# Optimization experiments

Measured on AMD Instinct MI355X. Metric: run time of the kernel, lower is better.

Reference implementation:

```python
import jax, jax.numpy as jnp
import numpy as np

B, S, H, E, V, OOV = 64, 400, 512, 256, 50000, 100

def setup_inputs() -> dict:
    key = jax.random.key(0)
    ks = jax.random.split(key, 32)
    p = lambda i, shape: jax.random.normal(ks[i], shape, jnp.float32) * 0.02
    emb = p(0, (V, E)).at[0].set(0.0)  # padding_idx=0
    return dict(
        summaries_in=jax.random.randint(ks[1], (B,), 1, V),
        h0=jax.random.normal(ks[2], (B, H), jnp.float32),
        c0=jax.random.normal(ks[3], (B, H), jnp.float32),
        encoder_out=jax.random.normal(ks[4], (B, S, 2 * H), jnp.float32),
        encoder_features=jax.random.normal(ks[5], (S * B, 2 * H), jnp.float32),
        encoder_mask=jnp.ones((S, B), jnp.float32),
        context=jax.random.normal(ks[6], (B, 2 * H), jnp.float32),
        coverage=jax.random.uniform(ks[7], (S, B), jnp.float32) * 0.01,
        texts_extended=jax.random.randint(ks[8], (S, B), 0, V + OOV),
        oov_size=OOV,
        emb=emb,
        W_feat=p(10, (2 * H, 2 * H)), b_feat=p(11, (2 * H,)),
        W_cov=p(12, (2 * H,)), b_cov=p(13, (2 * H,)),
        w_att=p(14, (2 * H,)), b_att=p(15, ()),
        W_ih=p(16, (4 * H, E)), W_hh=p(17, (4 * H, H)),
        b_ih=p(18, (4 * H,)), b_hh=p(19, (4 * H,)),
        W_ctx=p(20, (E, 2 * H + E)), b_ctx=p(21, (E,)),
        W_pg=p(22, (4 * H + E,)), b_pg=p(23, ()),
        W_o1=p(24, (H, 3 * H)), b_o1=p(25, (H,)),
        W_o2=p(26, (V, H)), b_o2=p(27, (V,)),
    )


def reference(summaries_in, h0, c0, encoder_out, encoder_features, encoder_mask,
              context, coverage, texts_extended, oov_size, emb,
              W_feat, b_feat, W_cov, b_cov, w_att, b_att,
              W_ih, W_hh, b_ih, b_hh, W_ctx, b_ctx, W_pg, b_pg,
              W_o1, b_o1, W_o2, b_o2):
    # embedding + context projection: [B, 2H+E] -> [B, E]
    x = emb[summaries_in]
    ctx_out = jnp.concatenate([context, x], axis=1) @ W_ctx.T + b_ctx
    # single LSTM step (torch gate order i, f, g, o)
    gates = ctx_out @ W_ih.T + b_ih + h0 @ W_hh.T + b_hh
    i, f, g, o = jnp.split(gates, 4, axis=1)
    c = jax.nn.sigmoid(f) * c0 + jax.nn.sigmoid(i) * jnp.tanh(g)
    h = jax.nn.sigmoid(o) * jnp.tanh(c)
    hidden_out = jnp.concatenate([h, c], axis=1)  # [B, 2H]
    # Bahdanau attention with coverage
    dec_feat = hidden_out @ W_feat.T + b_feat                 # [B, 2H]
    ef = encoder_features.reshape(S, B, 2 * H)                # [S, B, 2H]
    cov_feat = coverage[..., None] * W_cov + b_cov            # Linear(1, 2H)
    e = jnp.tanh(ef + dec_feat[None] + cov_feat) @ w_att + b_att  # [S, B]
    a = jax.nn.softmax(e, axis=0) * encoder_mask
    a = a / jnp.sum(a, axis=0, keepdims=True)                 # renormalize (Normalize(0))
    ctx_new = jnp.einsum('sb,bsd->bd', a, encoder_out)        # [B, 2H]
    coverage_next = coverage + a
    # pointer-generator mix
    gen_in = jnp.concatenate([ctx_new, hidden_out, ctx_out], axis=1)  # [B, 4H+E]
    p_gen = jax.nn.sigmoid(gen_in @ W_pg + b_pg)[:, None]             # [B, 1]
    logits = (jnp.concatenate([h, ctx_new], axis=1) @ W_o1.T + b_o1) @ W_o2.T + b_o2
    vocab_dist = p_gen * jax.nn.softmax(logits, axis=1)       # [B, V]
    attn_w = (1.0 - p_gen) * a.T                              # [B, S]
    vd = jnp.concatenate([vocab_dist, jnp.zeros((B, oov_size), vocab_dist.dtype)], axis=1)
    vd = vd.at[jnp.arange(B)[:, None], texts_extended.T].add(attn_w)  # scatter_add copy dist
    return vd, hidden_out, ctx_new, a, coverage_next
```

## Files before the change

kernel.cpp:

```cpp
#include <hip/hip_runtime.h>
#include <cmath>

#define B 64
#define S 400
#define H 512
#define E 256
#define V 50000
#define OOV 100
#define H2 1024
#define VDN (V + OOV)
#define NBLK_V 782

typedef __attribute__((ext_vector_type(8))) short short8;
typedef __attribute__((ext_vector_type(4))) float f32x4;

__device__ __forceinline__ float wred_sum(float v) {
#pragma unroll
  for (int o = 32; o > 0; o >>= 1) v += __shfl_down(v, o, 64);
  return v;
}
__device__ __forceinline__ float wred_max(float v) {
#pragma unroll
  for (int o = 32; o > 0; o >>= 1) v = fmaxf(v, __shfl_down(v, o, 64));
  return v;
}
__device__ __forceinline__ short f2bf(float f) {
  return __builtin_bit_cast(short, (__bf16)f);
}

__global__ __launch_bounds__(256) void k_init(const float* __restrict__ b_ctx,
                                              const float* __restrict__ b_ih,
                                              const float* __restrict__ b_hh,
                                              const float* __restrict__ b_feat,
                                              const float* __restrict__ b_o1,
                                              float* __restrict__ ctxoutT4,
                                              float* __restrict__ gates,
                                              float* __restrict__ dfeat,
                                              float* __restrict__ innerT4) {
  int idx = blockIdx.x * 256 + threadIdx.x;
  if (idx < 16384) {
    int j = ((idx >> 8) << 2) + (idx & 3);
    ctxoutT4[idx] = b_ctx[j];
  } else if (idx < 16384 + 131072) {
    int i = idx - 16384;
    int j = i & 2047;
    gates[i] = b_ih[j] + b_hh[j];
  } else if (idx < 16384 + 131072 + 65536) {
    int i = idx - 16384 - 131072;
    dfeat[i] = b_feat[i & 1023];
  } else {
    int i = idx - 16384 - 131072 - 65536;
    int j = ((i >> 8) << 2) + (i & 3);
    innerT4[i] = b_o1[j];
  }
}

__global__ __launch_bounds__(256) void k_pack(const float* __restrict__ context,
                                              const float* __restrict__ emb,
                                              const int* __restrict__ sumin,
                                              const float* __restrict__ h0,
                                              float* __restrict__ catT4,
                                              float* __restrict__ h0T4) {
  int idx = blockIdx.x * 256 + threadIdx.x;
  if (idx < 81920) {
    int e = idx & 3, b = (idx >> 2) & 63, q = idx >> 8;
    int k = q * 4 + e;
    catT4[idx] = (k < 1024) ? context[b * 1024 + k]
                            : emb[(size_t)sumin[b] * 256 + (k - 1024)];
  } else {
    int i = idx - 81920;
    int e = i & 3, b = (i >> 2) & 63, q = i >> 8;
    h0T4[i] = h0[b * 512 + q * 4 + e];
  }
}

template <int R, int KC, int OUTMODE>
__global__ __launch_bounds__(256) void k_gemmsk(
    const float* __restrict__ A1, const float* __restrict__ W1, int ldw1, int s1,
    const float* __restrict__ A2, const float* __restrict__ W2, int ldw2,
    float* __restrict__ out, int ldout) {
  const int lane = threadIdx.x;
  const int w = threadIdx.y;
  const int j0 = blockIdx.x * (4 * R) + w * R;
  const float* A;
  const float* W;
  int ldw, kc0;
  if ((int)blockIdx.y < s1) {
    A = A1; W = W1; ldw = ldw1; kc0 = blockIdx.y * KC;
  } else {
    A = A2; W = W2; ldw = ldw2; kc0 = (blockIdx.y - s1) * KC;
  }
  float acc[R];
#pragma unroll
  for (int r = 0; r < R; ++r) acc[r] = 0.f;
  const float* ap = A + (size_t)kc0 * 256 + lane * 4;
  const float* wr[R];
#pragma unroll
  for (int r = 0; r < R; ++r) wr[r] = W + (size_t)(j0 + r) * ldw + kc0 * 4;
#pragma unroll 8
  for (int k4 = 0; k4 < KC; ++k4) {
    float4 av = *(const float4*)(ap + (size_t)k4 * 256);
#pragma unroll
    for (int r = 0; r < R; ++r) {
      float4 wv = *(const float4*)(wr[r] + k4 * 4);
      acc[r] += av.x * wv.x + av.y * wv.y + av.z * wv.z + av.w * wv.w;
    }
  }
#pragma unroll
  for (int r = 0; r < R; ++r) {
    int j = j0 + r;
    if constexpr (OUTMODE == 0)
      atomicAdd(&out[((size_t)(j >> 2) * 64 + lane) * 4 + (j & 3)], acc[r]);
    else
      atomicAdd(&out[(size_t)lane * ldout + j], acc[r]);
  }
}

__global__ __launch_bounds__(256) void k_lstm(const float* __restrict__ gates,
                                              const float* __restrict__ c0,
                                              float* __restrict__ hidden,
                                              float* __restrict__ hcT4) {
  int idx = blockIdx.x * 256 + threadIdx.x;
  int b = idx >> 9, u = idx & 511;
  float gi = gates[(size_t)b * 2048 + u];
  float gf = gates[(size_t)b * 2048 + 512 + u];
  float gg = gates[(size_t)b * 2048 + 1024 + u];
  float go = gates[(size_t)b * 2048 + 1536 + u];
  float si = 1.f / (1.f + expf(-gi));
  float sf = 1.f / (1.f + expf(-gf));
  float so = 1.f / (1.f + expf(-go));
  float c = sf * c0[(size_t)b * 512 + u] + si * tanhf(gg);
  float h = so * tanhf(c);
  hidden[(size_t)b * H2 + u] = h;
  hidden[(size_t)b * H2 + 512 + u] = c;
  hcT4[((u >> 2) * 64 + b) * 4 + (u & 3)] = h;
  int k = 512 + u;
  hcT4[((k >> 2) * 64 + b) * 4 + (k & 3)] = c;
}

__global__ __launch_bounds__(128) void k_e(
    const float* __restrict__ ef, const float* __restrict__ dfeat,
    const float* __restrict__ cov, const float* __restrict__ Wcov,
    const float* __restrict__ bcov, const float* __restrict__ watt,
    const float* __restrict__ batt, float* __restrict__ e_out) {
  const int sb = blockIdx.x;
  const int b = sb & 63;
  const float cval = cov[sb];
  const float4* efr = (const float4*)(ef + (size_t)sb * H2);
  const float4* dfr = (const float4*)(dfeat + (size_t)b * H2);
  const float4* wcr = (const float4*)Wcov;
  const float4* bcr = (const float4*)bcov;
  const float4* war = (const float4*)watt;
  float sum = 0.f;
#pragma unroll
  for (int i = 0; i < 2; ++i) {
    int d4 = threadIdx.x + i * 128;
    float4 ev = efr[d4], dv = dfr[d4], wc = wcr[d4], bc = bcr[d4], wa = war[d4];
    sum += tanhf(ev.x + dv.x + cval * wc.x + bc.x) * wa.x;
    sum += tanhf(ev.y + dv.y + cval * wc.y + bc.y) * wa.y;
    sum += tanhf(ev.z + dv.z + cval * wc.z + bc.z) * wa.z;
    sum += tanhf(ev.w + dv.w + cval * wc.w + bc.w) * wa.w;
  }
  sum = wred_sum(sum);
  __shared__ float ls[2];
  if ((threadIdx.x & 63) == 0) ls[threadIdx.x >> 6] = sum;
  __syncthreads();
  if (threadIdx.x == 0) e_out[sb] = ls[0] + ls[1] + batt[0];
}

__global__ __launch_bounds__(512) void k_soft(const float* __restrict__ e,
                                              const float* __restrict__ mask,
                                              const float* __restrict__ cov_in,
                                              float* __restrict__ a_out,
                                              float* __restrict__ cov_out) {
  const int b = blockIdx.x;
  const int s = threadIdx.x;
  __shared__ float red[8];
  float ev = (s < S) ? e[s * B + b] : -INFINITY;
  float m = wred_max(ev);
  if ((s & 63) == 0) red[s >> 6] = m;
  __syncthreads();
  if (s == 0) {
    float mm = red[0];
#pragma unroll
    for (int i = 1; i < 8; ++i) mm = fmaxf(mm, red[i]);
    red[0] = mm;
  }
  __syncthreads();
  m = red[0];
  float ex = (s < S) ? mask[s * B + b] * expf(ev - m) : 0.f;
  float ws = wred_sum(ex);
  __syncthreads();
  if ((s & 63) == 0) red[s >> 6] = ws;
  __syncthreads();
  if (s == 0) {
    float z = 0.f;
#pragma unroll
    for (int i = 0; i < 8; ++i) z += red[i];
    red[0] = z;
  }
  __syncthreads();
  float Z = red[0];
  if (s < S) {
    float av = ex / Z;
    a_out[s * B + b] = av;
    cov_out[s * B + b] = cov_in[s * B + b] + av;
  }
}

__global__ __launch_bounds__(256) void k_ctxp(const float* __restrict__ a,
                                              const float* __restrict__ enc,
                                              float* __restrict__ part) {
  const int b = blockIdx.x & 63;
  const int sc = blockIdx.x >> 6;
  const int d = threadIdx.x * 4;
  float4 acc = make_float4(0.f, 0.f, 0.f, 0.f);
  for (int s = sc * 25; s < sc * 25 + 25; ++s) {
    float av = a[s * B + b];
    float4 ev = *(const float4*)(enc + ((size_t)b * S + s) * H2 + d);
    acc.x += av * ev.x;
    acc.y += av * ev.y;
    acc.z += av * ev.z;
    acc.w += av * ev.w;
  }
  *(float4*)(part + (size_t)blockIdx.x * H2 + d) = acc;
}

__global__ __launch_bounds__(256) void k_ctxred(const float* __restrict__ part,
                                                float* __restrict__ ctx_new,
                                                float* __restrict__ ctxT4) {
  int idx = blockIdx.x * 256 + threadIdx.x;
  float s = 0.f;
#pragma unroll
  for (int sc = 0; sc < 16; ++sc) s += part[(size_t)sc * 65536 + idx];
  int b = idx >> 10, d = idx & 1023;
  ctx_new[idx] = s;
  ctxT4[((d >> 2) * 64 + b) * 4 + (d & 3)] = s;
}

__global__ __launch_bounds__(256) void k_pgen(
    const float* __restrict__ ctx_new, const float* __restrict__ hidden,
    const float* __restrict__ ctxoutT4, const float* __restrict__ Wpg,
    const float* __restrict__ bpg, float* __restrict__ pgen) {
  const int b = blockIdx.x;
  float p = 0.f;
  for (int k = threadIdx.x; k < 2304; k += 256) {
    float v;
    if (k < 1024) v = ctx_new[(size_t)b * H2 + k];
    else if (k < 2048) v = hidden[(size_t)b * H2 + k - 1024];
    else {
      int ko = k - 2048;
      v = ctxoutT4[((ko >> 2) * 64 + b) * 4 + (ko & 3)];
    }
    p += v * Wpg[k];
  }
  p = wred_sum(p);
  __shared__ float red[4];
  if ((threadIdx.x & 63) == 0) red[threadIdx.x >> 6] = p;
  __syncthreads();
  if (threadIdx.x == 0) {
    float d = red[0] + red[1] + red[2] + red[3] + bpg[0];
    pgen[b] = 1.f / (1.f + expf(-d));
  }
}

__global__ __launch_bounds__(256) void k_packinner(const float* __restrict__ innerT4,
                                                   short8* __restrict__ packB) {
  int f = blockIdx.x * 256 + threadIdx.x;
  int l = f & 63, bt = (f >> 6) & 3, ks = f >> 8;
  int b = bt * 16 + (l & 15);
  int kbase = ks * 32 + (l >> 4) * 8;
  float4 q0 = *(const float4*)&innerT4[(size_t)(kbase / 4) * 256 + b * 4];
  float4 q1 = *(const float4*)&innerT4[(size_t)(kbase / 4 + 1) * 256 + b * 4];
  short8 frag;
  frag[0] = f2bf(q0.x); frag[1] = f2bf(q0.y);
  frag[2] = f2bf(q0.z); frag[3] = f2bf(q0.w);
  frag[4] = f2bf(q1.x); frag[5] = f2bf(q1.y);
  frag[6] = f2bf(q1.z); frag[7] = f2bf(q1.w);
  packB[f] = frag;
}

__global__ __launch_bounds__(256) void k_mfma_logits(
    const float* __restrict__ W2, const short8* __restrict__ packB,
    const float* __restrict__ bias, float* __restrict__ logits,
    float* __restrict__ mp, float* __restrict__ zp) {
  const int l = threadIdx.x;
  const int w = threadIdx.y;
  const int jblk = blockIdx.x * 64;
  const int jw = jblk + w * 16;
  const int jv = min(jw + (l & 15), V - 1);
  const float* wp = W2 + (size_t)jv * 512 + (l >> 4) * 8;

  f32x4 acc0 = {0.f, 0.f, 0.f, 0.f}, acc1 = acc0, acc2 = acc0, acc3 = acc0;
#pragma unroll 2
  for (int ks = 0; ks < 16; ++ks) {
    float4 w0 = *(const float4*)&wp[ks * 32];
    float4 w1 = *(const float4*)&wp[ks * 32 + 4];
    short8 af;
    af[0] = f2bf(w0.x); af[1] = f2bf(w0.y); af[2] = f2bf(w0.z); af[3] = f2bf(w0.w);
    af[4] = f2bf(w1.x); af[5] = f2bf(w1.y); af[6] = f2bf(w1.z); af[7] = f2bf(w1.w);
    short8 b0 = packB[(ks * 4 + 0) * 64 + l];
    short8 b1 = packB[(ks * 4 + 1) * 64 + l];
    short8 b2 = packB[(ks * 4 + 2) * 64 + l];
    short8 b3 = packB[(ks * 4 + 3) * 64 + l];
    acc0 = __builtin_amdgcn_mfma_f32_16x16x32_bf16(af, b0, acc0, 0, 0, 0);
    acc1 = __builtin_amdgcn_mfma_f32_16x16x32_bf16(af, b1, acc1, 0, 0, 0);
    acc2 = __builtin_amdgcn_mfma_f32_16x16x32_bf16(af, b2, acc2, 0, 0, 0);
    acc3 = __builtin_amdgcn_mfma_f32_16x16x32_bf16(af, b3, acc3, 0, 0, 0);
  }

  __shared__ float tile[64][65];
  const int rbase = w * 16 + (l >> 4) * 4;
#pragma unroll
  for (int v = 0; v < 4; ++v) {
    int jl = rbase + v;
    int j = jblk + jl;
    float bv = bias[min(j, V - 1)];
    bool valid = (j < V);
    tile[jl][0 * 16 + (l & 15)] = valid ? acc0[v] + bv : -INFINITY;
    tile[jl][1 * 16 + (l & 15)] = valid ? acc1[v] + bv : -INFINITY;
    tile[jl][2 * 16 + (l & 15)] = valid ? acc2[v] + bv : -INFINITY;
    tile[jl][3 * 16 + (l & 15)] = valid ? acc3[v] + bv : -INFINITY;
  }
  __syncthreads();
  const int t = w * 64 + l;
#pragma unroll
  for (int i = 0; i < 16; ++i) {
    int idx = i * 256 + t;
    int jl = idx & 63;
    int b = idx >> 6;
    int j = jblk + jl;
    if (j < V) logits[(size_t)b * V + j] = tile[jl][b];
  }
  if (t < 64) {
    float m = -INFINITY;
#pragma unroll
    for (int jl = 0; jl < 64; ++jl) m = fmaxf(m, tile[jl][t]);
    float z = 0.f;
#pragma unroll
    for (int jl = 0; jl < 64; ++jl) z += expf(tile[jl][t] - m);
    mp[(size_t)blockIdx.x * 64 + t] = m;
    zp[(size_t)blockIdx.x * 64 + t] = z;
  }
}

__global__ __launch_bounds__(256) void k_vdm(const float* __restrict__ logits,
                                             const float* __restrict__ mp,
                                             const float* __restrict__ zp,
                                             const float* __restrict__ pgen,
                                             float* __restrict__ out) {
  const int b = blockIdx.x >> 3;
  const int c = blockIdx.x & 7;
  const int t = threadIdx.x;
  __shared__ float red[4];
  float m = -INFINITY;
  for (int i = t; i < NBLK_V; i += 256) m = fmaxf(m, mp[i * 64 + b]);
  m = wred_max(m);
  if ((t & 63) == 0) red[t >> 6] = m;
  __syncthreads();
  const float M = fmaxf(fmaxf(red[0], red[1]), fmaxf(red[2], red[3]));
  float z = 0.f;
  for (int i = t; i < NBLK_V; i += 256) z += zp[i * 64 + b] * expf(mp[i * 64 + b] - M);
  z = wred_sum(z);
  __syncthreads();
  if ((t & 63) == 0) red[t >> 6] = z;
  __syncthreads();
  const float Z = red[0] + red[1] + red[2] + red[3];
  const float scale = pgen[b] / Z;
  const int v0 = c * 6272;
  const int v1 = min(v0 + 6272, VDN);
  for (int v = v0 + t; v < v1; v += 256) {
    float val = (v < V) ? scale * expf(logits[(size_t)b * V + v] - M) : 0.f;
    out[(size_t)b * VDN + v] = val;
  }
}

__global__ __launch_bounds__(256) void k_scatter(const float* __restrict__ a,
                                                 const int* __restrict__ tex,
                                                 const float* __restrict__ pgen,
                                                 float* __restrict__ vd) {
  int g = blockIdx.x * 256 + threadIdx.x;
  if (g >= S * B) return;
  int b = g & 63;
  float w = (1.f - pgen[b]) * a[g];
  atomicAdd(&vd[(size_t)b * VDN + tex[g]], w);
}

extern "C" void kernel_launch(void* const* d_in, const int* in_sizes, int n_in,
                              void* d_out, int out_size, void* d_ws, size_t ws_size,
                              hipStream_t stream) {
  const int* sumin = (const int*)d_in[0];
  const float* h0 = (const float*)d_in[1];
  const float* c0 = (const float*)d_in[2];
  const float* enc_out = (const float*)d_in[3];
  const float* ef = (const float*)d_in[4];
  const float* mask = (const float*)d_in[5];
  const float* context = (const float*)d_in[6];
  const float* coverage = (const float*)d_in[7];
  const int* tex = (const int*)d_in[8];
  const float* emb = (const float*)d_in[10];
  const float* W_feat = (const float*)d_in[11];
  const float* b_feat = (const float*)d_in[12];
  const float* W_cov = (const float*)d_in[13];
  const float* b_cov = (const float*)d_in[14];
  const float* w_att = (const float*)d_in[15];
  const float* b_att = (const float*)d_in[16];
  const float* W_ih = (const float*)d_in[17];
  const float* W_hh = (const float*)d_in[18];
  const float* b_ih = (const float*)d_in[19];
  const float* b_hh = (const float*)d_in[20];
  const float* W_ctx = (const float*)d_in[21];
  const float* b_ctx = (const float*)d_in[22];
  const float* W_pg = (const float*)d_in[23];
  const float* b_pg = (const float*)d_in[24];
  const float* W_o1 = (const float*)d_in[25];
  const float* b_o1 = (const float*)d_in[26];
  const float* W_o2 = (const float*)d_in[27];
  const float* b_o2 = (const float*)d_in[28];

  float* out = (float*)d_out;
  float* vd = out;
  float* hidden = vd + (size_t)B * VDN;
  float* ctx_new = hidden + (size_t)B * H2;
  float* a_out = ctx_new + (size_t)B * H2;
  float* cov_out = a_out + (size_t)S * B;

  float* ws = (float*)d_ws;
  float* catT4 = ws;
  float* h0T4 = catT4 + 81920;
  float* ctxoutT4 = h0T4 + 32768;
  float* gates = ctxoutT4 + 16384;
  float* hidcatT4 = gates + 131072;
  float* dfeat = hidcatT4 + 65536;
  float* e_ws = dfeat + 65536;
  float* ctxnewT4 = e_ws + 25600;
  float* innerT4 = ctxnewT4 + 65536;
  float* pgen = innerT4 + 32768;
  float* mp = pgen + 64;
  float* zp = mp + 50048;
  float* packBf = zp + 50048;
  float* logits = packBf + 16384;
  float* part = logits;
  short8* packB = (short8*)packBf;

  dim3 gblk(64, 4);

  k_init<<<960, 256, 0, stream>>>(b_ctx, b_ih, b_hh, b_feat, b_o1, ctxoutT4,
                                  gates, dfeat, innerT4);
  k_pack<<<448, 256, 0, stream>>>(context, emb, sumin, h0, catT4, h0T4);
  k_gemmsk<2, 64, 0><<<dim3(32, 5), gblk, 0, stream>>>(
      catT4, W_ctx, 1280, 5, nullptr, nullptr, 0, ctxoutT4, 0);
  k_gemmsk<2, 64, 1><<<dim3(256, 3), gblk, 0, stream>>>(
      ctxoutT4, W_ih, 256, 1, h0T4, W_hh, 512, gates, 2048);
  k_lstm<<<128, 256, 0, stream>>>(gates, c0, hidden, hidcatT4);
  k_gemmsk<2, 64, 1><<<dim3(128, 4), gblk, 0, stream>>>(
      hidcatT4, W_feat, 1024, 4, nullptr, nullptr, 0, dfeat, 1024);
  k_e<<<S * B, 128, 0, stream>>>(ef, dfeat, coverage, W_cov, b_cov, w_att, b_att, e_ws);
  k_soft<<<B, 512, 0, stream>>>(e_ws, mask, coverage, a_out, cov_out);
  k_ctxp<<<16 * B, 256, 0, stream>>>(a_out, enc_out, part);
  k_ctxred<<<256, 256, 0, stream>>>(part, ctx_new, ctxnewT4);
  k_pgen<<<B, 256, 0, stream>>>(ctx_new, hidden, ctxoutT4, W_pg, b_pg, pgen);
  k_gemmsk<2, 64, 0><<<dim3(64, 6), gblk, 0, stream>>>(
      hidcatT4, W_o1, 1536, 2, ctxnewT4, W_o1 + 512, 1536, innerT4, 0);
  k_packinner<<<16, 256, 0, stream>>>(innerT4, packB);
  k_mfma_logits<<<NBLK_V, gblk, 0, stream>>>(W_o2, packB, b_o2, logits, mp, zp);
  k_vdm<<<B * 8, 256, 0, stream>>>(logits, mp, zp, pgen, vd);
  k_scatter<<<100, 256, 0, stream>>>(a_out, tex, pgen, vd);
}
```

Measured before the change: 223.4 us.

## Merge init/pack kernels, batch attention rows, split ctx over more chunks, prefetch W2

```diff
diff --git a/kernel.cpp b/kernel.cpp
--- a/kernel.cpp
+++ b/kernel.cpp
@@ -10,6 +10,7 @@
 #define H2 1024
 #define VDN (V + OOV)
 #define NBLK_V 782
+#define SC 40
 
 typedef __attribute__((ext_vector_type(8))) short short8;
 typedef __attribute__((ext_vector_type(4))) float f32x4;
@@ -28,15 +29,15 @@
   return __builtin_bit_cast(short, (__bf16)f);
 }
 
-__global__ __launch_bounds__(256) void k_init(const float* __restrict__ b_ctx,
-                                              const float* __restrict__ b_ih,
-                                              const float* __restrict__ b_hh,
-                                              const float* __restrict__ b_feat,
-                                              const float* __restrict__ b_o1,
-                                              float* __restrict__ ctxoutT4,
-                                              float* __restrict__ gates,
-                                              float* __restrict__ dfeat,
-                                              float* __restrict__ innerT4) {
+__global__ __launch_bounds__(256) void k_pre(
+    const float* __restrict__ b_ctx, const float* __restrict__ b_ih,
+    const float* __restrict__ b_hh, const float* __restrict__ b_feat,
+    const float* __restrict__ b_o1, const float* __restrict__ context,
+    const float* __restrict__ emb, const int* __restrict__ sumin,
+    const float* __restrict__ h0, float* __restrict__ ctxoutT4,
+    float* __restrict__ gates, float* __restrict__ dfeat,
+    float* __restrict__ innerT4, float* __restrict__ catT4,
+    float* __restrict__ h0T4) {
   int idx = blockIdx.x * 256 + threadIdx.x;
   if (idx < 16384) {
     int j = ((idx >> 8) << 2) + (idx & 3);
@@ -48,27 +49,18 @@
   } else if (idx < 16384 + 131072 + 65536) {
     int i = idx - 16384 - 131072;
     dfeat[i] = b_feat[i & 1023];
-  } else {
+  } else if (idx < 245760) {
     int i = idx - 16384 - 131072 - 65536;
     int j = ((i >> 8) << 2) + (i & 3);
     innerT4[i] = b_o1[j];
-  }
-}
-
-__global__ __launch_bounds__(256) void k_pack(const float* __restrict__ context,
-                                              const float* __restrict__ emb,
-                                              const int* __restrict__ sumin,
-                                              const float* __restrict__ h0,
-                                              float* __restrict__ catT4,
-                                              float* __restrict__ h0T4) {
-  int idx = blockIdx.x * 256 + threadIdx.x;
-  if (idx < 81920) {
-    int e = idx & 3, b = (idx >> 2) & 63, q = idx >> 8;
+  } else if (idx < 245760 + 81920) {
+    int i = idx - 245760;
+    int e = i & 3, b = (i >> 2) & 63, q = i >> 8;
     int k = q * 4 + e;
-    catT4[idx] = (k < 1024) ? context[b * 1024 + k]
-                            : emb[(size_t)sumin[b] * 256 + (k - 1024)];
+    catT4[i] = (k < 1024) ? context[b * 1024 + k]
+                          : emb[(size_t)sumin[b] * 256 + (k - 1024)];
   } else {
-    int i = idx - 81920;
+    int i = idx - 245760 - 81920;
     int e = i & 3, b = (i >> 2) & 63, q = i >> 8;
     h0T4[i] = h0[b * 512 + q * 4 + e];
   }
@@ -138,12 +130,15 @@
   hcT4[((k >> 2) * 64 + b) * 4 + (k & 3)] = c;
 }
 
-__global__ __launch_bounds__(128) void k_e(
+__global__ __launch_bounds__(256) void k_e(
     const float* __restrict__ ef, const float* __restrict__ dfeat,
     const float* __restrict__ cov, const float* __restrict__ Wcov,
     const float* __restrict__ bcov, const float* __restrict__ watt,
     const float* __restrict__ batt, float* __restrict__ e_out) {
-  const int sb = blockIdx.x;
+  const int t = threadIdx.x;
+  const int r = t >> 5;
+  const int li = t & 31;
+  const int sb = blockIdx.x * 8 + r;
   const int b = sb & 63;
   const float cval = cov[sb];
   const float4* efr = (const float4*)(ef + (size_t)sb * H2);
@@ -153,19 +148,17 @@
   const float4* war = (const float4*)watt;
   float sum = 0.f;
 #pragma unroll
-  for (int i = 0; i < 2; ++i) {
-    int d4 = threadIdx.x + i * 128;
+  for (int i = 0; i < 8; ++i) {
+    int d4 = li + i * 32;
     float4 ev = efr[d4], dv = dfr[d4], wc = wcr[d4], bc = bcr[d4], wa = war[d4];
     sum += tanhf(ev.x + dv.x + cval * wc.x + bc.x) * wa.x;
     sum += tanhf(ev.y + dv.y + cval * wc.y + bc.y) * wa.y;
     sum += tanhf(ev.z + dv.z + cval * wc.z + bc.z) * wa.z;
     sum += tanhf(ev.w + dv.w + cval * wc.w + bc.w) * wa.w;
   }
-  sum = wred_sum(sum);
-  __shared__ float ls[2];
-  if ((threadIdx.x & 63) == 0) ls[threadIdx.x >> 6] = sum;
-  __syncthreads();
-  if (threadIdx.x == 0) e_out[sb] = ls[0] + ls[1] + batt[0];
+#pragma unroll
+  for (int o = 16; o > 0; o >>= 1) sum += __shfl_down(sum, o, 32);
+  if (li == 0) e_out[sb] = sum + batt[0];
 }
 
 __global__ __launch_bounds__(512) void k_soft(const float* __restrict__ e,
@@ -215,7 +208,9 @@
   const int sc = blockIdx.x >> 6;
   const int d = threadIdx.x * 4;
   float4 acc = make_float4(0.f, 0.f, 0.f, 0.f);
-  for (int s = sc * 25; s < sc * 25 + 25; ++s) {
+#pragma unroll
+  for (int i = 0; i < 10; ++i) {
+    int s = sc * 10 + i;
     float av = a[s * B + b];
     float4 ev = *(const float4*)(enc + ((size_t)b * S + s) * H2 + d);
     acc.x += av * ev.x;
@@ -232,7 +227,7 @@
   int idx = blockIdx.x * 256 + threadIdx.x;
   float s = 0.f;
 #pragma unroll
-  for (int sc = 0; sc < 16; ++sc) s += part[(size_t)sc * 65536 + idx];
+  for (int sc = 0; sc < SC; ++sc) s += part[(size_t)sc * 65536 + idx];
   int b = idx >> 10, d = idx & 1023;
   ctx_new[idx] = s;
   ctxT4[((d >> 2) * 64 + b) * 4 + (d & 3)] = s;
@@ -289,16 +284,17 @@
   const int jblk = blockIdx.x * 64;
   const int jw = jblk + w * 16;
   const int jv = min(jw + (l & 15), V - 1);
-  const float* wp = W2 + (size_t)jv * 512 + (l >> 4) * 8;
+  const float4* wp4 = (const float4*)(W2 + (size_t)jv * 512 + (l >> 4) * 8);
 
   f32x4 acc0 = {0.f, 0.f, 0.f, 0.f}, acc1 = acc0, acc2 = acc0, acc3 = acc0;
-#pragma unroll 2
+  float4 cw0 = wp4[0], cw1 = wp4[1];
+#pragma unroll
   for (int ks = 0; ks < 16; ++ks) {
-    float4 w0 = *(const float4*)&wp[ks * 32];
-    float4 w1 = *(const float4*)&wp[ks * 32 + 4];
+    float4 nw0, nw1;
+    if (ks < 15) { nw0 = wp4[(ks + 1) * 8]; nw1 = wp4[(ks + 1) * 8 + 1]; }
     short8 af;
-    af[0] = f2bf(w0.x); af[1] = f2bf(w0.y); af[2] = f2bf(w0.z); af[3] = f2bf(w0.w);
-    af[4] = f2bf(w1.x); af[5] = f2bf(w1.y); af[6] = f2bf(w1.z); af[7] = f2bf(w1.w);
+    af[0] = f2bf(cw0.x); af[1] = f2bf(cw0.y); af[2] = f2bf(cw0.z); af[3] = f2bf(cw0.w);
+    af[4] = f2bf(cw1.x); af[5] = f2bf(cw1.y); af[6] = f2bf(cw1.z); af[7] = f2bf(cw1.w);
     short8 b0 = packB[(ks * 4 + 0) * 64 + l];
     short8 b1 = packB[(ks * 4 + 1) * 64 + l];
     short8 b2 = packB[(ks * 4 + 2) * 64 + l];
@@ -307,6 +303,7 @@
     acc1 = __builtin_amdgcn_mfma_f32_16x16x32_bf16(af, b1, acc1, 0, 0, 0);
     acc2 = __builtin_amdgcn_mfma_f32_16x16x32_bf16(af, b2, acc2, 0, 0, 0);
     acc3 = __builtin_amdgcn_mfma_f32_16x16x32_bf16(af, b3, acc3, 0, 0, 0);
+    if (ks < 15) { cw0 = nw0; cw1 = nw1; }
   }
 
   __shared__ float tile[64][65];
@@ -445,9 +442,9 @@
 
   dim3 gblk(64, 4);
 
-  k_init<<<960, 256, 0, stream>>>(b_ctx, b_ih, b_hh, b_feat, b_o1, ctxoutT4,
-                                  gates, dfeat, innerT4);
-  k_pack<<<448, 256, 0, stream>>>(context, emb, sumin, h0, catT4, h0T4);
+  k_pre<<<1408, 256, 0, stream>>>(b_ctx, b_ih, b_hh, b_feat, b_o1, context, emb,
+                                  sumin, h0, ctxoutT4, gates, dfeat, innerT4,
+                                  catT4, h0T4);
   k_gemmsk<2, 64, 0><<<dim3(32, 5), gblk, 0, stream>>>(
       catT4, W_ctx, 1280, 5, nullptr, nullptr, 0, ctxoutT4, 0);
   k_gemmsk<2, 64, 1><<<dim3(256, 3), gblk, 0, stream>>>(
@@ -455,9 +452,10 @@
   k_lstm<<<128, 256, 0, stream>>>(gates, c0, hidden, hidcatT4);
   k_gemmsk<2, 64, 1><<<dim3(128, 4), gblk, 0, stream>>>(
       hidcatT4, W_feat, 1024, 4, nullptr, nullptr, 0, dfeat, 1024);
-  k_e<<<S * B, 128, 0, stream>>>(ef, dfeat, coverage, W_cov, b_cov, w_att, b_att, e_ws);
+  k_e<<<3200, 256, 0, stream>>>(ef, dfeat, coverage, W_cov, b_cov, w_att, b_att,
+                                e_ws);
   k_soft<<<B, 512, 0, stream>>>(e_ws, mask, coverage, a_out, cov_out);
-  k_ctxp<<<16 * B, 256, 0, stream>>>(a_out, enc_out, part);
+  k_ctxp<<<SC * B, 256, 0, stream>>>(a_out, enc_out, part);
   k_ctxred<<<256, 256, 0, stream>>>(part, ctx_new, ctxnewT4);
   k_pgen<<<B, 256, 0, stream>>>(ctx_new, hidden, ctxoutT4, W_pg, b_pg, pgen);
   k_gemmsk<2, 64, 0><<<dim3(64, 6), gblk, 0, stream>>>(
```

New measurement: 231.7 us. 1.04x slower.
